# Kernel optimization log

Measured on AMD Instinct MI355X. Metric: run time of the kernel, lower is better.

The kernel has to match this reference:

```python
import jax, jax.numpy as jnp
import numpy as np

WIN = 8     # sliding-chunk window size (Long2DSCSelfAttention default w=8)
HEADS = 8   # num_heads


def setup_inputs() -> dict:
    key = jax.random.key(0)
    ks = jax.random.split(key, 3)
    B, C, H, W = 4, 512, 64, 64
    x = jax.random.normal(ks[0], (B, C, H, W), jnp.float32)
    w_qkv = jax.random.normal(ks[1], (3 * C, C), jnp.float32) * 0.02
    b_qkv = jnp.zeros((3 * C,), jnp.float32)
    w_proj = jax.random.normal(ks[2], (C, C), jnp.float32) * 0.02
    b_proj = jnp.zeros((C,), jnp.float32)
    return {"x": x, "w_qkv": w_qkv, "b_qkv": b_qkv, "w_proj": w_proj, "b_proj": b_proj}


def _chunk(t, nh, nw, win):
    B, _, _, h, d = t.shape
    t = t.reshape(B, nh, win, nw, win, h, d)
    return t.transpose(0, 5, 1, 3, 2, 4, 6).reshape(B, h, nh, nw, win * win, d)


def reference(x, w_qkv, b_qkv, w_proj, b_proj):
    B, C, H, W = x.shape
    win, heads = WIN, HEADS
    d = C // heads
    nh, nw = H // win, W // win
    m = win * win  # tokens per chunk

    xf = x.transpose(0, 2, 3, 1)                      # [B,H,W,C]
    qkv = xf @ w_qkv.T + b_qkv                        # [B,H,W,3C]
    qkv = qkv.reshape(B, H, W, 3, heads, d)
    q = _chunk(qkv[..., 0, :, :], nh, nw, win)        # [B,h,nh,nw,m,d]
    k = _chunk(qkv[..., 1, :, :], nh, nw, win)
    v = _chunk(qkv[..., 2, :, :], nh, nw, win)

    # pad chunk grid by one chunk on each side; gather 3x3 chunk neighborhoods
    kp = jnp.pad(k, ((0, 0), (0, 0), (1, 1), (1, 1), (0, 0), (0, 0)))
    vp = jnp.pad(v, ((0, 0), (0, 0), (1, 1), (1, 1), (0, 0), (0, 0)))
    k9 = jnp.concatenate([kp[:, :, i:i + nh, j:j + nw] for i in range(3) for j in range(3)], axis=4)  # [B,h,nh,nw,9m,d]
    v9 = jnp.concatenate([vp[:, :, i:i + nh, j:j + nw] for i in range(3) for j in range(3)], axis=4)

    # validity mask for neighbor chunks at the image boundary
    valid = jnp.pad(jnp.ones((nh, nw), bool), ((1, 1), (1, 1)))
    vmask = jnp.concatenate(
        [jnp.repeat(valid[i:i + nh, j:j + nw][..., None], m, axis=-1) for i in range(3) for j in range(3)],
        axis=-1)                                      # [nh,nw,9m]

    scale = float(d) ** -0.5
    attn = jnp.einsum('bhxyqd,bhxykd->bhxyqk', q * scale, k9)      # [B,h,nh,nw,m,9m]
    neg = jnp.asarray(-1e9, attn.dtype)
    attn = jnp.where(vmask[None, None, :, :, None, :], attn, neg)
    attn = jax.nn.softmax(attn, axis=-1)
    out = jnp.einsum('bhxyqk,bhxykd->bhxyqd', attn, v9)            # [B,h,nh,nw,m,d]

    out = out.reshape(B, heads, nh, nw, win, win, d)
    out = out.transpose(0, 2, 4, 3, 5, 1, 6).reshape(B, H, W, C)
    out = out @ w_proj.T + b_proj
    return out.transpose(0, 3, 1, 2)                               # [B,C,H,W]
```

## Files before the change

kernel.cpp:

```cpp
#include <hip/hip_runtime.h>
#include <cstdint>
#include <cstddef>

namespace {

constexpr int kC = 512;
constexpr int kHW = 4096;
constexpr int kHeads = 8;
constexpr int kChunkElems = 64 * 64;

typedef float f32x4 __attribute__((ext_vector_type(4)));
typedef _Float16 f16x8 __attribute__((ext_vector_type(8)));
union FragU { uint4 u; f16x8 h; };

__device__ __forceinline__ ushort f16rn(float x) {
  _Float16 h = (_Float16)x;
  ushort u;
  __builtin_memcpy(&u, &h, 2);
  return u;
}
__device__ __forceinline__ uint pack2(ushort a, ushort b) {
  return (uint)a | ((uint)b << 16);
}
__device__ __forceinline__ float fexp2(float x) {
  return exp2f(x);
}
__device__ __forceinline__ uint pkrtz(float a, float b) {
  auto h = __builtin_amdgcn_cvt_pkrtz(a, b);
  uint u;
  __builtin_memcpy(&u, &h, 4);
  return u;
}
__device__ __forceinline__ void gld16(const void* g, void* lds) {
  __builtin_amdgcn_global_load_lds(
      (const __attribute__((address_space(1))) uint32_t*)g,
      (__attribute__((address_space(3))) uint32_t*)lds, 16, 0, 0);
}

__global__ __launch_bounds__(256)
void convw16_kernel(const float* __restrict__ wqkv, ushort* __restrict__ wqh,
                    const float* __restrict__ wproj, ushort* __restrict__ wph)
{
  const int bx = blockIdx.x;
  const float* src;
  ushort* dst;
  int idx;
  if (bx < 384) { src = wqkv; dst = wqh; idx = (bx * 256 + threadIdx.x) * 8; }
  else { src = wproj; dst = wph; idx = ((bx - 384) * 256 + threadIdx.x) * 8; }
  float4 v0 = *(const float4*)(src + idx);
  float4 v1 = *(const float4*)(src + idx + 4);
  float xs[8] = {v0.x, v0.y, v0.z, v0.w, v1.x, v1.y, v1.z, v1.w};
  ushort hh[8];
#pragma unroll
  for (int e = 0; e < 8; ++e) hh[e] = f16rn(xs[e]);
  *(uint4*)(dst + idx) = make_uint4(pack2(hh[0], hh[1]), pack2(hh[2], hh[3]),
                                    pack2(hh[4], hh[5]), pack2(hh[6], hh[7]));
}

__global__ __launch_bounds__(256)
void convx_kernel(const float* __restrict__ x, ushort* __restrict__ xt)
{
  __shared__ float LT[64][68];
  const int tid = threadIdx.x;
  const int t0 = blockIdx.x * 64;
  const int c0 = blockIdx.y * 64;
  const int b  = blockIdx.z;
  const float* xb = x + (size_t)b * kC * kHW;

#pragma unroll
  for (int u = 0; u < 4; ++u) {
    int idx = tid + u * 256;
    int rc = idx >> 4;
    int t4 = (idx & 15) << 2;
    float4 val = *(const float4*)(xb + (size_t)(c0 + rc) * kHW + t0 + t4);
    LT[t4 + 0][rc] = val.x;
    LT[t4 + 1][rc] = val.y;
    LT[t4 + 2][rc] = val.z;
    LT[t4 + 3][rc] = val.w;
  }
  __syncthreads();
#pragma unroll
  for (int u = 0; u < 4; ++u) {
    int idx = tid + u * 256;
    int rt = idx >> 4;
    int c4 = (idx & 15) << 2;
    float4 v = *(const float4*)&LT[rt][c4];
    size_t o = ((size_t)b * kHW + t0 + rt) * kC + c0 + c4;
    *(ushort4*)(xt + o) = make_ushort4(f16rn(v.x), f16rn(v.y),
                                       f16rn(v.z), f16rn(v.w));
  }
}

__global__ __launch_bounds__(256)
void qkv_mfma_kernel(const ushort* __restrict__ xt,
                     const ushort* __restrict__ wq,
                     const float* __restrict__ bqkv,
                     ushort* __restrict__ qo, ushort* __restrict__ ko,
                     ushort* __restrict__ vo)
{
  __shared__ __align__(16) ushort As[2][128 * 64];
  __shared__ __align__(16) ushort Bs[2][128 * 64];

  const int tid  = threadIdx.x;
  const int lane = tid & 63;
  const int wv   = tid >> 6;
  const int quad = lane >> 4;
  const int l15  = lane & 15;
  const int wm = wv & 1, wn = wv >> 1;
  const int m0 = blockIdx.x * 128;
  const int n0 = blockIdx.y * 128;
  const int b  = blockIdx.z;

  const ushort* xb = xt + (size_t)b * kHW * kC;

  auto stage = [&](int buf, int k0) {
#pragma unroll
    for (int ii = 0; ii < 4; ++ii) {
      int i = wv * 4 + ii;
      int m = i * 8 + (lane >> 3);
      int gch = (lane & 7) ^ (m & 7);
      size_t goA = (size_t)(m0 + m) * kC + k0 + gch * 8;
      gld16(xb + goA, (char*)&As[buf][0] + i * 1024);
      size_t goB = (size_t)(n0 + m) * kC + k0 + gch * 8;
      gld16(wq + goB, (char*)&Bs[buf][0] + i * 1024);
    }
  };

  f32x4 acc[4][4];
#pragma unroll
  for (int i = 0; i < 4; ++i)
#pragma unroll
    for (int j = 0; j < 4; ++j) acc[i][j] = (f32x4){0.f, 0.f, 0.f, 0.f};

  stage(0, 0);
  asm volatile("s_waitcnt vmcnt(0)" ::: "memory");
  asm volatile("s_barrier" ::: "memory");

  for (int kt = 0; kt < 8; ++kt) {
    const int cur = kt & 1;
    if (kt < 7) stage(cur ^ 1, (kt + 1) * 64);

    const ushort* Ac = &As[cur][0];
    const ushort* Bc = &Bs[cur][0];
#pragma unroll
    for (int s = 0; s < 2; ++s) {
      const int gq = s * 4 + quad;
      FragU aA[4], bB[4];
#pragma unroll
      for (int mi = 0; mi < 4; ++mi) {
        int mr = wm * 64 + mi * 16 + l15;
        int off = mr * 64 + ((gq ^ (mr & 7)) * 8);
        aA[mi].u = *(const uint4*)&Ac[off];
      }
#pragma unroll
      for (int ni = 0; ni < 4; ++ni) {
        int nr = wn * 64 + ni * 16 + l15;
        int off = nr * 64 + ((gq ^ (nr & 7)) * 8);
        bB[ni].u = *(const uint4*)&Bc[off];
      }
#pragma unroll
      for (int mi = 0; mi < 4; ++mi)
#pragma unroll
        for (int ni = 0; ni < 4; ++ni)
          acc[mi][ni] = __builtin_amdgcn_mfma_f32_16x16x32_f16(aA[mi].h, bB[ni].h, acc[mi][ni], 0, 0, 0);
    }

    asm volatile("s_waitcnt lgkmcnt(0)" ::: "memory");
    if (kt < 7) asm volatile("s_waitcnt vmcnt(0)" ::: "memory");
    asm volatile("s_barrier" ::: "memory");
  }

  const int sec = n0 >> 9;
  const int jwbase = n0 + wn * 64;
  const int head = (jwbase >> 6) & 7;
  const size_t hbb = ((size_t)b * kHeads + head) * 64;
  float biasv[4];
#pragma unroll
  for (int ni = 0; ni < 4; ++ni) biasv[ni] = bqkv[jwbase + ni * 16 + l15];

  if (sec == 2) {
#pragma unroll
    for (int ni = 0; ni < 4; ++ni) {
      int dd = ni * 16 + l15;
#pragma unroll
      for (int mi = 0; mi < 4; ++mi) {
        int t0t = m0 + wm * 64 + mi * 16 + quad * 4;
        int h = t0t >> 6, w = t0t & 63;
        int cy = h >> 3, iy = h & 7, cx = w >> 3, ix = w & 7;
        size_t cb = (hbb + cy * 8 + cx) * (size_t)kChunkElems;
        int tokb = iy * 8 + ix;
        ushort hh[4];
#pragma unroll
        for (int r = 0; r < 4; ++r) hh[r] = f16rn(acc[mi][ni][r] + biasv[ni]);
        *(ushort4*)(vo + cb + (size_t)dd * 64 + tokb) = make_ushort4(hh[0], hh[1], hh[2], hh[3]);
      }
    }
  } else {
    ushort* dst = (sec == 0) ? qo : ko;
    const float sc = (sec == 0) ? 0.125f * 1.44269504089f : 1.0f;
    ushort* tH = &As[0][0] + wv * 1152;
    const int ltok = lane >> 2;
    const int dd0 = (lane & 3) * 16;
#pragma unroll
    for (int mi = 0; mi < 4; ++mi) {
#pragma unroll
      for (int ni = 0; ni < 4; ++ni)
#pragma unroll
        for (int r = 0; r < 4; ++r)
          tH[(quad * 4 + r) * 68 + ni * 16 + l15] =
              f16rn((acc[mi][ni][r] + biasv[ni]) * sc);
      int tg = m0 + wm * 64 + mi * 16 + ltok;
      int h = tg >> 6, w = tg & 63;
      int cy = h >> 3, iy = h & 7, cx = w >> 3, ix = w & 7;
      size_t cb = (hbb + cy * 8 + cx) * (size_t)kChunkElems
                + (size_t)(iy * 8 + ix) * 64 + dd0;
      uint4 h0 = *(const uint4*)&tH[ltok * 68 + dd0];
      uint4 h1 = *(const uint4*)&tH[ltok * 68 + dd0 + 8];
      *(uint4*)(dst + cb) = h0;
      *(uint4*)(dst + cb + 8) = h1;
    }
  }
}

__global__ __launch_bounds__(256)
void attn_mfma_kernel(const ushort* __restrict__ qg, const ushort* __restrict__ kg,
                      const ushort* __restrict__ vg,
                      ushort* __restrict__ ao)
{
  __shared__ __align__(16) ushort KB[4096], VB[4096];
  __shared__ __align__(16) ushort Ps[4 * 16 * 72];

  const int tid  = threadIdx.x;
  const int lane = tid & 63;
  const int wv   = tid >> 6;
  const int quad = lane >> 4;
  const int l15  = lane & 15;

  const int bx = blockIdx.x;
  const int g  = (bx & 7) * 4 + ((bx >> 3) >> 6);
  const int c  = (bx >> 3) & 63;
  const int b = g >> 3, head = g & 7;
  const int cy = c >> 3, cx = c & 7;

  const size_t hb = (size_t)b * kHeads + head;
  const size_t gbase = hb * 64 * (size_t)kChunkElems;
  const size_t cbase = gbase + (size_t)c * (size_t)kChunkElems;

  FragU aQ0, aQ1;
  {
    const ushort* qr = qg + cbase + (size_t)(wv * 16 + l15) * 64 + quad * 8;
    aQ0.u = *(const uint4*)(qr);
    aQ1.u = *(const uint4*)(qr + 32);
  }

  const int boff = ((lane >> 3) * 64) + (((lane & 7) ^ (lane >> 3)) * 8);
  const ushort* kgB = kg + gbase + boff + (size_t)(wv * 2) * 512;
  const ushort* vgB = vg + gbase + boff + (size_t)(wv * 2) * 512;
  char* kDst0 = (char*)KB + (wv * 2) * 1024;
  char* vDst0 = (char*)VB + (wv * 2) * 1024;

  int kvOff0[4], kvOff1[4];
  {
    const int sw = l15 & 7;
#pragma unroll
    for (int nt = 0; nt < 4; ++nt) {
      int row = nt * 16 + l15;
      kvOff0[nt] = row * 64 + ((quad ^ sw) * 8);
      kvOff1[nt] = row * 64 + (((4 + quad) ^ sw) * 8);
    }
  }

  ushort* PsW = Ps + wv * 1152;
  ushort* pWr = PsW + l15 * 72 + quad * 4;
  const ushort* pRd = PsW + l15 * 72 + quad * 8;

  unsigned long long list = 0ull;
  int cnt = 0;
#pragma unroll
  for (int p = 0; p < 9; ++p) {
    const int dy = p / 3 - 1, dx = p % 3 - 1;
    int ny = cy + dy, nx = cx + dx;
    if ((unsigned)ny < 8u && (unsigned)nx < 8u) {
      list |= (unsigned long long)(ny * 8 + nx) << (6 * cnt);
      ++cnt;
    }
  }

  f32x4 o[4];
#pragma unroll
  for (int r = 0; r < 4; ++r) o[r] = (f32x4){0.f, 0.f, 0.f, 0.f};
  float rsum = 0.f;

  {
    int ch0 = (int)(list & 63);
    const ushort* pk = kgB + (size_t)ch0 * kChunkElems;
    gld16(pk, kDst0);
    gld16(pk + 512, kDst0 + 1024);
    const ushort* pv = vgB + (size_t)ch0 * kChunkElems;
    gld16(pv, vDst0);
    gld16(pv + 512, vDst0 + 1024);
  }

  for (int i = 0; i < cnt; ++i) {
    const bool more = (i + 1 < cnt);
    const int chn = (int)((list >> (6 * (i + 1))) & 63);

    asm volatile("s_waitcnt vmcnt(2)" ::: "memory");
    asm volatile("s_barrier" ::: "memory");

    FragU kf[8];
#pragma unroll
    for (int nt = 0; nt < 4; ++nt) {
      kf[nt * 2].u     = *(const uint4*)&KB[kvOff0[nt]];
      kf[nt * 2 + 1].u = *(const uint4*)&KB[kvOff1[nt]];
    }
    asm volatile("s_waitcnt lgkmcnt(0)" ::: "memory");
    asm volatile("s_waitcnt vmcnt(0)" ::: "memory");
    asm volatile("s_barrier" ::: "memory");

    if (more) {
      const ushort* pk = kgB + (size_t)chn * kChunkElems;
      gld16(pk, kDst0);
      gld16(pk + 512, kDst0 + 1024);
    }

    f32x4 s[4];
#pragma unroll
    for (int nt = 0; nt < 4; ++nt) s[nt] = (f32x4){0.f, 0.f, 0.f, 0.f};
#pragma unroll
    for (int nt = 0; nt < 4; ++nt) {
      s[nt] = __builtin_amdgcn_mfma_f32_16x16x32_f16(kf[nt * 2].h, aQ0.h, s[nt], 0, 0, 0);
      s[nt] = __builtin_amdgcn_mfma_f32_16x16x32_f16(kf[nt * 2 + 1].h, aQ1.h, s[nt], 0, 0, 0);
    }

#pragma unroll
    for (int nt = 0; nt < 4; ++nt) {
      float e0 = fexp2(s[nt][0]);
      float e1 = fexp2(s[nt][1]);
      float e2 = fexp2(s[nt][2]);
      float e3 = fexp2(s[nt][3]);
      rsum += (e0 + e1) + (e2 + e3);
      *(uint2*)(pWr + nt * 16) = make_uint2(pkrtz(e0, e1), pkrtz(e2, e3));
    }

    FragU aP0, aP1;
    aP0.u = *(const uint4*)(pRd);
    aP1.u = *(const uint4*)(pRd + 32);

#pragma unroll
    for (int nt = 0; nt < 4; ++nt) {
      FragU v0, v1;
      v0.u = *(const uint4*)&VB[kvOff0[nt]];
      v1.u = *(const uint4*)&VB[kvOff1[nt]];
      o[nt] = __builtin_amdgcn_mfma_f32_16x16x32_f16(v0.h, aP0.h, o[nt], 0, 0, 0);
      o[nt] = __builtin_amdgcn_mfma_f32_16x16x32_f16(v1.h, aP1.h, o[nt], 0, 0, 0);
    }

    asm volatile("s_waitcnt lgkmcnt(0)" ::: "memory");
    asm volatile("s_barrier" ::: "memory");
    if (more) {
      const ushort* pv = vgB + (size_t)chn * kChunkElems;
      gld16(pv, vDst0);
      gld16(pv + 512, vDst0 + 1024);
    }
  }

  rsum += __shfl_xor(rsum, 16, 64);
  rsum += __shfl_xor(rsum, 32, 64);
  const float inv = 1.0f / rsum;

  const int trg = wv * 16 + l15;
  const int hp = cy * 8 + (trg >> 3);
  const int wp = cx * 8 + (trg & 7);
  const size_t obase = ((size_t)b * kHW + hp * 64 + wp) * (size_t)kC + head * 64;

#pragma unroll
  for (int nt = 0; nt < 4; ++nt) {
    float v0 = o[nt][0] * inv;
    float v1 = o[nt][1] * inv;
    float v2 = o[nt][2] * inv;
    float v3 = o[nt][3] * inv;
    *(ushort4*)(ao + obase + nt * 16 + quad * 4) =
        make_ushort4(f16rn(v0), f16rn(v1), f16rn(v2), f16rn(v3));
  }
}

__global__ __launch_bounds__(256)
void proj_mfma_kernel(const ushort* __restrict__ ao,
                      const ushort* __restrict__ wp,
                      const float* __restrict__ bproj,
                      float* __restrict__ out)
{
  __shared__ __align__(16) ushort As[2][128 * 64];
  __shared__ __align__(16) ushort Bs[2][128 * 64];

  const int tid  = threadIdx.x;
  const int lane = tid & 63;
  const int wv   = tid >> 6;
  const int quad = lane >> 4;
  const int l15  = lane & 15;
  const int wm = wv & 1, wn = wv >> 1;
  const int n0g = blockIdx.x * 128;
  const int m0  = blockIdx.y * 128;
  const int b   = n0g >> 12;
  const int tl0 = n0g & 4095;

  auto stage = [&](int buf, int k0) {
#pragma unroll
    for (int ii = 0; ii < 4; ++ii) {
      int i = wv * 4 + ii;
      int m = i * 8 + (lane >> 3);
      int gch = (lane & 7) ^ (m & 7);
      size_t goA = (size_t)(m0 + m) * kC + k0 + gch * 8;
      gld16(wp + goA, (char*)&As[buf][0] + i * 1024);
      size_t goB = (size_t)(n0g + m) * kC + k0 + gch * 8;
      gld16(ao + goB, (char*)&Bs[buf][0] + i * 1024);
    }
  };

  f32x4 acc[4][4];
#pragma unroll
  for (int i = 0; i < 4; ++i)
#pragma unroll
    for (int j = 0; j < 4; ++j) acc[i][j] = (f32x4){0.f, 0.f, 0.f, 0.f};

  stage(0, 0);
  asm volatile("s_waitcnt vmcnt(0)" ::: "memory");
  asm volatile("s_barrier" ::: "memory");

  for (int kt = 0; kt < 8; ++kt) {
    const int cur = kt & 1;
    if (kt < 7) stage(cur ^ 1, (kt + 1) * 64);

    const ushort* Ac = &As[cur][0];
    const ushort* Bc = &Bs[cur][0];
#pragma unroll
    for (int s = 0; s < 2; ++s) {
      const int gq = s * 4 + quad;
      FragU aA[4], bB[4];
#pragma unroll
      for (int mi = 0; mi < 4; ++mi) {
        int mr = wm * 64 + mi * 16 + l15;
        int off = mr * 64 + ((gq ^ (mr & 7)) * 8);
        aA[mi].u = *(const uint4*)&Ac[off];
      }
#pragma unroll
      for (int ni = 0; ni < 4; ++ni) {
        int nr = wn * 64 + ni * 16 + l15;
        int off = nr * 64 + ((gq ^ (nr & 7)) * 8);
        bB[ni].u = *(const uint4*)&Bc[off];
      }
#pragma unroll
      for (int mi = 0; mi < 4; ++mi)
#pragma unroll
        for (int ni = 0; ni < 4; ++ni)
          acc[mi][ni] = __builtin_amdgcn_mfma_f32_16x16x32_f16(aA[mi].h, bB[ni].h, acc[mi][ni], 0, 0, 0);
    }

    asm volatile("s_waitcnt lgkmcnt(0)" ::: "memory");
    if (kt < 7) asm volatile("s_waitcnt vmcnt(0)" ::: "memory");
    asm volatile("s_barrier" ::: "memory");
  }

#pragma unroll
  for (int mi = 0; mi < 4; ++mi)
#pragma unroll
    for (int r = 0; r < 4; ++r) {
      int c = m0 + wm * 64 + mi * 16 + quad * 4 + r;
      float bias = bproj[c];
      size_t rowb = ((size_t)b * kC + c) * (size_t)kHW + tl0 + wn * 64;
#pragma unroll
      for (int ni = 0; ni < 4; ++ni)
        out[rowb + ni * 16 + l15] = acc[mi][ni][r] + bias;
    }
}

}

extern "C" void kernel_launch(void* const* d_in, const int* in_sizes, int n_in,
                              void* d_out, int out_size, void* d_ws, size_t ws_size,
                              hipStream_t stream)
{
  const float* x     = (const float*)d_in[0];
  const float* wqkv  = (const float*)d_in[1];
  const float* bqkv  = (const float*)d_in[2];
  const float* wproj = (const float*)d_in[3];
  const float* bproj = (const float*)d_in[4];
  float* out = (float*)d_out;

  const size_t seg = (size_t)2048 * kChunkElems;
  ushort* base = (ushort*)d_ws;
  ushort* qb = base + 0 * seg;
  ushort* kb = base + 1 * seg;
  ushort* vb = base + 2 * seg;
  ushort* xt = base + 3 * seg;
  ushort* ao = xt;
  ushort* wp16 = base + 4 * seg;
  ushort* wqh = base + 5 * seg;

  convw16_kernel<<<dim3(512), 256, 0, stream>>>(wqkv, wqh, wproj, wp16);
  convx_kernel<<<dim3(64, 8, 4), 256, 0, stream>>>(x, xt);
  qkv_mfma_kernel<<<dim3(32, 12, 4), 256, 0, stream>>>(xt, wqh, bqkv,
                                                       qb, kb, vb);
  attn_mfma_kernel<<<dim3(2048), 256, 0, stream>>>(qb, kb, vb, ao);
  proj_mfma_kernel<<<dim3(128, 4), 256, 0, stream>>>(ao, wp16, bproj, out);
}
```

Before: 190.3 us.

## Single-buffer LDS in QKV and proj GEMMs, prefetching from registers

Replaces the double-buffered shared-memory tiles in the QKV and output-projection GEMM kernels with single buffers. Each k-step first loads the whole tile's fragments into registers, then issues the next global-to-LDS stage, then runs the MFMAs from registers. This halves LDS use per block (64KB to 32KB), which may allow more resident blocks per CU. In exchange it needs more fragment registers and adds a second barrier per iteration.

```diff
diff --git a/kernel.cpp b/kernel.cpp
--- a/kernel.cpp
+++ b/kernel.cpp
@@ -98,8 +98,8 @@
                      ushort* __restrict__ qo, ushort* __restrict__ ko,
                      ushort* __restrict__ vo)
 {
-  __shared__ __align__(16) ushort As[2][128 * 64];
-  __shared__ __align__(16) ushort Bs[2][128 * 64];
+  __shared__ __align__(16) ushort As[128 * 64];
+  __shared__ __align__(16) ushort Bs[128 * 64];
 
   const int tid  = threadIdx.x;
   const int lane = tid & 63;
@@ -113,16 +113,14 @@
 
   const ushort* xb = xt + (size_t)b * kHW * kC;
 
-  auto stage = [&](int buf, int k0) {
+  auto stage = [&](int k0) {
 #pragma unroll
     for (int ii = 0; ii < 4; ++ii) {
       int i = wv * 4 + ii;
       int m = i * 8 + (lane >> 3);
       int gch = (lane & 7) ^ (m & 7);
-      size_t goA = (size_t)(m0 + m) * kC + k0 + gch * 8;
-      gld16(xb + goA, (char*)&As[buf][0] + i * 1024);
-      size_t goB = (size_t)(n0 + m) * kC + k0 + gch * 8;
-      gld16(wq + goB, (char*)&Bs[buf][0] + i * 1024);
+      gld16(xb + (size_t)(m0 + m) * kC + k0 + gch * 8, (char*)As + i * 1024);
+      gld16(wq + (size_t)(n0 + m) * kC + k0 + gch * 8, (char*)Bs + i * 1024);
     }
   };
 
@@ -132,42 +130,42 @@
 #pragma unroll
     for (int j = 0; j < 4; ++j) acc[i][j] = (f32x4){0.f, 0.f, 0.f, 0.f};
 
-  stage(0, 0);
-  asm volatile("s_waitcnt vmcnt(0)" ::: "memory");
-  asm volatile("s_barrier" ::: "memory");
+  stage(0);
 
   for (int kt = 0; kt < 8; ++kt) {
-    const int cur = kt & 1;
-    if (kt < 7) stage(cur ^ 1, (kt + 1) * 64);
-
-    const ushort* Ac = &As[cur][0];
-    const ushort* Bc = &Bs[cur][0];
-#pragma unroll
-    for (int s = 0; s < 2; ++s) {
-      const int gq = s * 4 + quad;
-      FragU aA[4], bB[4];
-#pragma unroll
-      for (int mi = 0; mi < 4; ++mi) {
-        int mr = wm * 64 + mi * 16 + l15;
-        int off = mr * 64 + ((gq ^ (mr & 7)) * 8);
-        aA[mi].u = *(const uint4*)&Ac[off];
-      }
-#pragma unroll
-      for (int ni = 0; ni < 4; ++ni) {
-        int nr = wn * 64 + ni * 16 + l15;
-        int off = nr * 64 + ((gq ^ (nr & 7)) * 8);
-        bB[ni].u = *(const uint4*)&Bc[off];
-      }
-#pragma unroll
-      for (int mi = 0; mi < 4; ++mi)
-#pragma unroll
-        for (int ni = 0; ni < 4; ++ni)
-          acc[mi][ni] = __builtin_amdgcn_mfma_f32_16x16x32_f16(aA[mi].h, bB[ni].h, acc[mi][ni], 0, 0, 0);
-    }
-
+    asm volatile("s_waitcnt vmcnt(0)" ::: "memory");
+    asm volatile("s_barrier" ::: "memory");
+
+    FragU a0[4], a1[4], b0[4], b1[4];
+#pragma unroll
+    for (int mi = 0; mi < 4; ++mi) {
+      int mr = wm * 64 + mi * 16 + l15;
+      int sw = mr & 7;
+      a0[mi].u = *(const uint4*)&As[mr * 64 + ((quad ^ sw) * 8)];
+      a1[mi].u = *(const uint4*)&As[mr * 64 + (((4 + quad) ^ sw) * 8)];
+    }
+#pragma unroll
+    for (int ni = 0; ni < 4; ++ni) {
+      int nr = wn * 64 + ni * 16 + l15;
+      int sw = nr & 7;
+      b0[ni].u = *(const uint4*)&Bs[nr * 64 + ((quad ^ sw) * 8)];
+      b1[ni].u = *(const uint4*)&Bs[nr * 64 + (((4 + quad) ^ sw) * 8)];
+    }
     asm volatile("s_waitcnt lgkmcnt(0)" ::: "memory");
-    if (kt < 7) asm volatile("s_waitcnt vmcnt(0)" ::: "memory");
-    asm volatile("s_barrier" ::: "memory");
+    asm volatile("s_barrier" ::: "memory");
+
+    if (kt < 7) stage((kt + 1) * 64);
+
+#pragma unroll
+    for (int mi = 0; mi < 4; ++mi)
+#pragma unroll
+      for (int ni = 0; ni < 4; ++ni)
+        acc[mi][ni] = __builtin_amdgcn_mfma_f32_16x16x32_f16(a0[mi].h, b0[ni].h, acc[mi][ni], 0, 0, 0);
+#pragma unroll
+    for (int mi = 0; mi < 4; ++mi)
+#pragma unroll
+      for (int ni = 0; ni < 4; ++ni)
+        acc[mi][ni] = __builtin_amdgcn_mfma_f32_16x16x32_f16(a1[mi].h, b1[ni].h, acc[mi][ni], 0, 0, 0);
   }
 
   const int sec = n0 >> 9;
@@ -198,7 +196,7 @@
   } else {
     ushort* dst = (sec == 0) ? qo : ko;
     const float sc = (sec == 0) ? 0.125f * 1.44269504089f : 1.0f;
-    ushort* tH = &As[0][0] + wv * 1152;
+    ushort* tH = As + wv * 1152;
     const int ltok = lane >> 2;
     const int dd0 = (lane & 3) * 16;
 #pragma unroll
@@ -391,8 +389,8 @@
                       const float* __restrict__ bproj,
                       float* __restrict__ out)
 {
-  __shared__ __align__(16) ushort As[2][128 * 64];
-  __shared__ __align__(16) ushort Bs[2][128 * 64];
+  __shared__ __align__(16) ushort As[128 * 64];
+  __shared__ __align__(16) ushort Bs[128 * 64];
 
   const int tid  = threadIdx.x;
   const int lane = tid & 63;
@@ -405,16 +403,14 @@
   const int b   = n0g >> 12;
   const int tl0 = n0g & 4095;
 
-  auto stage = [&](int buf, int k0) {
+  auto stage = [&](int k0) {
 #pragma unroll
     for (int ii = 0; ii < 4; ++ii) {
       int i = wv * 4 + ii;
       int m = i * 8 + (lane >> 3);
       int gch = (lane & 7) ^ (m & 7);
-      size_t goA = (size_t)(m0 + m) * kC + k0 + gch * 8;
-      gld16(wp + goA, (char*)&As[buf][0] + i * 1024);
-      size_t goB = (size_t)(n0g + m) * kC + k0 + gch * 8;
-      gld16(ao + goB, (char*)&Bs[buf][0] + i * 1024);
+      gld16(wp + (size_t)(m0 + m) * kC + k0 + gch * 8, (char*)As + i * 1024);
+      gld16(ao + (size_t)(n0g + m) * kC + k0 + gch * 8, (char*)Bs + i * 1024);
     }
   };
 
@@ -424,42 +420,42 @@
 #pragma unroll
     for (int j = 0; j < 4; ++j) acc[i][j] = (f32x4){0.f, 0.f, 0.f, 0.f};
 
-  stage(0, 0);
-  asm volatile("s_waitcnt vmcnt(0)" ::: "memory");
-  asm volatile("s_barrier" ::: "memory");
+  stage(0);
 
   for (int kt = 0; kt < 8; ++kt) {
-    const int cur = kt & 1;
-    if (kt < 7) stage(cur ^ 1, (kt + 1) * 64);
-
-    const ushort* Ac = &As[cur][0];
-    const ushort* Bc = &Bs[cur][0];
-#pragma unroll
-    for (int s = 0; s < 2; ++s) {
-      const int gq = s * 4 + quad;
-      FragU aA[4], bB[4];
-#pragma unroll
-      for (int mi = 0; mi < 4; ++mi) {
-        int mr = wm * 64 + mi * 16 + l15;
-        int off = mr * 64 + ((gq ^ (mr & 7)) * 8);
-        aA[mi].u = *(const uint4*)&Ac[off];
-      }
-#pragma unroll
-      for (int ni = 0; ni < 4; ++ni) {
-        int nr = wn * 64 + ni * 16 + l15;
-        int off = nr * 64 + ((gq ^ (nr & 7)) * 8);
-        bB[ni].u = *(const uint4*)&Bc[off];
-      }
-#pragma unroll
-      for (int mi = 0; mi < 4; ++mi)
-#pragma unroll
-        for (int ni = 0; ni < 4; ++ni)
-          acc[mi][ni] = __builtin_amdgcn_mfma_f32_16x16x32_f16(aA[mi].h, bB[ni].h, acc[mi][ni], 0, 0, 0);
-    }
-
+    asm volatile("s_waitcnt vmcnt(0)" ::: "memory");
+    asm volatile("s_barrier" ::: "memory");
+
+    FragU a0[4], a1[4], b0[4], b1[4];
+#pragma unroll
+    for (int mi = 0; mi < 4; ++mi) {
+      int mr = wm * 64 + mi * 16 + l15;
+      int sw = mr & 7;
+      a0[mi].u = *(const uint4*)&As[mr * 64 + ((quad ^ sw) * 8)];
+      a1[mi].u = *(const uint4*)&As[mr * 64 + (((4 + quad) ^ sw) * 8)];
+    }
+#pragma unroll
+    for (int ni = 0; ni < 4; ++ni) {
+      int nr = wn * 64 + ni * 16 + l15;
+      int sw = nr & 7;
+      b0[ni].u = *(const uint4*)&Bs[nr * 64 + ((quad ^ sw) * 8)];
+      b1[ni].u = *(const uint4*)&Bs[nr * 64 + (((4 + quad) ^ sw) * 8)];
+    }
     asm volatile("s_waitcnt lgkmcnt(0)" ::: "memory");
-    if (kt < 7) asm volatile("s_waitcnt vmcnt(0)" ::: "memory");
-    asm volatile("s_barrier" ::: "memory");
+    asm volatile("s_barrier" ::: "memory");
+
+    if (kt < 7) stage((kt + 1) * 64);
+
+#pragma unroll
+    for (int mi = 0; mi < 4; ++mi)
+#pragma unroll
+      for (int ni = 0; ni < 4; ++ni)
+        acc[mi][ni] = __builtin_amdgcn_mfma_f32_16x16x32_f16(a0[mi].h, b0[ni].h, acc[mi][ni], 0, 0, 0);
+#pragma unroll
+    for (int mi = 0; mi < 4; ++mi)
+#pragma unroll
+      for (int ni = 0; ni < 4; ++ni)
+        acc[mi][ni] = __builtin_amdgcn_mfma_f32_16x16x32_f16(a1[mi].h, b1[ni].h, acc[mi][ni], 0, 0, 0);
   }
 
 #pragma unroll
```

After: 176.9 us. 1.08x faster.
